# Kernel optimization log

Hardware: AMD Instinct MI355X
Metric: run time of the kernel (lower is better)

Reference implementation:

```python
import jax, jax.numpy as jnp
import numpy as np
import math

H = 768      # hidden_size
NH = 12      # num_head
DH = H // NH # head dim
FF = 4 * H
EPS = 1e-6

def _layernorm(x, g, b):
    mu = jnp.mean(x, axis=-1, keepdims=True)
    var = jnp.mean(jnp.square(x - mu), axis=-1, keepdims=True)
    return (x - mu) * jax.lax.rsqrt(var + EPS) * g + b

def setup_inputs() -> dict:
    key = jax.random.key(0)
    ks = jax.random.split(key, 16)
    B, N = 8, 1024
    xav = lambda k, i, o: jax.random.uniform(k, (i, o), jnp.float32, -1.0, 1.0) * math.sqrt(6.0 / (i + o))
    bias = lambda k, o: jax.random.normal(k, (o,), jnp.float32) * 1e-6
    return {
        "x": jax.random.normal(ks[0], (B, N, H), jnp.float32),
        "wq": xav(ks[1], H, H), "bq": bias(ks[2], H),
        "wk": xav(ks[3], H, H), "bk": bias(ks[4], H),
        "wv": xav(ks[5], H, H), "bv": bias(ks[6], H),
        "wo": xav(ks[7], H, H), "bo": bias(ks[8], H),
        "w1": xav(ks[9], H, FF), "b1": bias(ks[10], FF),
        "w2": xav(ks[11], FF, H), "b2": bias(ks[12], H),
        "g1": jnp.ones((H,), jnp.float32), "be1": jnp.zeros((H,), jnp.float32),
        "g2": jnp.ones((H,), jnp.float32), "be2": jnp.zeros((H,), jnp.float32),
    }

def reference(x, wq, bq, wk, bk, wv, bv, wo, bo, w1, b1, w2, b2, g1, be1, g2, be2):
    B, N, _ = x.shape
    x1 = _layernorm(x, g1, be1)
    # QKV projections -> (B, NH, N, DH)
    split = lambda t: t.reshape(B, N, NH, DH).transpose(0, 2, 1, 3)
    q = split(x1 @ wq + bq)
    k = split(x1 @ wk + bk)
    v = split(x1 @ wv + bv)
    # NOTE: original divides by sqrt(attention_size)=sqrt(H), not sqrt(DH)
    scores = jnp.einsum("bhqd,bhkd->bhqk", q, k) / math.sqrt(H)
    weights = jax.nn.softmax(scores, axis=-1)
    ctx = jnp.einsum("bhqk,bhkd->bhqd", weights, v)
    ctx = ctx.transpose(0, 2, 1, 3).reshape(B, N, H)
    attn_out = ctx @ wo + bo  # dropout is identity in eval
    x = x + attn_out
    x2 = _layernorm(x, g2, be2)
    h = jax.nn.gelu(x2 @ w1 + b1, approximate=False)  # torch F.gelu is exact erf gelu
    mlp_out = h @ w2 + b2
    x = x + mlp_out
    return (x, weights)
```

## Files before the change

kernel.cpp:

```cpp
#include <hip/hip_runtime.h>
#include <cstdint>
#include <cstddef>

#define H 768
#define NHEAD 12
#define DH 64
#define FFD 3072
#define BATCH 8
#define SEQ 1024
#define NTOK (BATCH*SEQ)
#define QKVS 2304

typedef __bf16 bf16x8 __attribute__((ext_vector_type(8)));
typedef float  floatx4 __attribute__((ext_vector_type(4)));

#define MFMA_BF16(a,b,c) __builtin_amdgcn_mfma_f32_16x16x32_bf16((a),(b),(c),0,0,0)

__device__ __forceinline__ void gload16(const void* g, void* l) {
    __builtin_amdgcn_global_load_lds((const __attribute__((address_space(1))) void*)g,
                                     (__attribute__((address_space(3))) void*)l,
                                     16, 0, 0);
}

__device__ __forceinline__ float gelu_erf(float x) {
    float z = fabsf(x) * 0.70710678118654752f;
    float t = __builtin_amdgcn_rcpf(1.0f + 0.3275911f * z);
    float poly = t * (0.254829592f +
               t * (-0.284496736f +
               t * (1.421413741f +
               t * (-1.453152027f +
               t * 1.061405429f))));
    float e = __expf(-z * z);
    float erfv = 1.0f - poly * e;
    erfv = copysignf(erfv, x);
    return 0.5f * x * (1.0f + erfv);
}

__global__ __launch_bounds__(256) void prep_kernel(
    const float* __restrict__ wq, const float* __restrict__ wk,
    const float* __restrict__ wv, const float* __restrict__ wo,
    const float* __restrict__ w1, const float* __restrict__ w2,
    const float* __restrict__ bq, const float* __restrict__ bk,
    const float* __restrict__ bv,
    __bf16* __restrict__ wqkvT, __bf16* __restrict__ woT,
    __bf16* __restrict__ w1T, __bf16* __restrict__ w2T,
    float* __restrict__ bqkv,
    const float* __restrict__ x, const float* __restrict__ g1,
    const float* __restrict__ be1, __bf16* __restrict__ x1b) {
    __shared__ float tile[32][33];
    int bid = blockIdx.x;
    int tid = threadIdx.x;
    if (bid < 6912) {
        const float* W; __bf16* T; int Kd, Nn, bx, by;
        if (bid < 1728) {
            int part = bid / 576;
            int rem = bid - part * 576;
            W = part == 0 ? wq : (part == 1 ? wk : wv);
            T = wqkvT + (size_t)part * H * H;
            Kd = H; Nn = H; bx = rem % 24; by = rem / 24;
        } else if (bid < 2304) {
            int rem = bid - 1728;
            W = wo; T = woT; Kd = H; Nn = H; bx = rem % 24; by = rem / 24;
        } else if (bid < 4608) {
            int rem = bid - 2304;
            W = w1; T = w1T; Kd = H; Nn = FFD; bx = rem % 96; by = rem / 96;
        } else {
            int rem = bid - 4608;
            W = w2; T = w2T; Kd = FFD; Nn = H; bx = rem % 24; by = rem / 24;
        }
        int tx = tid & 31, ty = tid >> 5;
        int n0 = bx * 32, k0 = by * 32;
#pragma unroll
        for (int i = 0; i < 32; i += 8)
            tile[ty + i][tx] = W[(size_t)(k0 + ty + i) * Nn + n0 + tx];
        __syncthreads();
#pragma unroll
        for (int i = 0; i < 32; i += 8)
            T[(size_t)(n0 + ty + i) * Kd + k0 + tx] = (__bf16)tile[tx][ty + i];
    } else if (bid < 6921) {
        int i = (bid - 6912) * 256 + tid;
        float v = i < H ? bq[i] : (i < 2 * H ? bk[i - H] : bv[i - 2 * H]);
        bqkv[i] = v;
    } else {
        int row  = (bid - 6921) * 4 + (tid >> 6);
        int lane = tid & 63;
        const float* xr = x + (size_t)row * H;
        float v[12];
        float s = 0.f;
#pragma unroll
        for (int i = 0; i < 12; i++) { v[i] = xr[lane + i * 64]; s += v[i]; }
#pragma unroll
        for (int m = 32; m >= 1; m >>= 1) s += __shfl_xor(s, m, 64);
        float mu = s * (1.0f / H);
        float q = 0.f;
#pragma unroll
        for (int i = 0; i < 12; i++) { float d = v[i] - mu; q += d * d; }
#pragma unroll
        for (int m = 32; m >= 1; m >>= 1) q += __shfl_xor(q, m, 64);
        float rstd = rsqrtf(q * (1.0f / H) + 1e-6f);
        __bf16* orow = x1b + (size_t)row * H;
#pragma unroll
        for (int i = 0; i < 12; i++) {
            int c = lane + i * 64;
            orow[c] = (__bf16)((v[i] - mu) * rstd * g1[c] + be1[c]);
        }
    }
}

__global__ __launch_bounds__(256) void ln_kernel(const float* __restrict__ x,
                                                 const float* __restrict__ g,
                                                 const float* __restrict__ be,
                                                 __bf16* __restrict__ out) {
    int row  = blockIdx.x * 4 + (threadIdx.x >> 6);
    int lane = threadIdx.x & 63;
    const float* xr = x + (size_t)row * H;
    float v[12];
    float s = 0.f;
#pragma unroll
    for (int i = 0; i < 12; i++) { v[i] = xr[lane + i * 64]; s += v[i]; }
#pragma unroll
    for (int m = 32; m >= 1; m >>= 1) s += __shfl_xor(s, m, 64);
    float mu = s * (1.0f / H);
    float q = 0.f;
#pragma unroll
    for (int i = 0; i < 12; i++) { float d = v[i] - mu; q += d * d; }
#pragma unroll
    for (int m = 32; m >= 1; m >>= 1) q += __shfl_xor(q, m, 64);
    float rstd = rsqrtf(q * (1.0f / H) + 1e-6f);
    __bf16* orow = out + (size_t)row * H;
#pragma unroll
    for (int i = 0; i < 12; i++) {
        int c = lane + i * 64;
        orow[c] = (__bf16)((v[i] - mu) * rstd * g[c] + be[c]);
    }
}

__global__ __launch_bounds__(256) void vtrans_kernel(const __bf16* __restrict__ qkv,
                                                     __bf16* __restrict__ vT) {
    __shared__ __bf16 tile[64][65];
    int b = blockIdx.z, h = blockIdx.y, n0 = blockIdx.x * 64;
    int tx = threadIdx.x, ty = threadIdx.y;
#pragma unroll
    for (int r = ty; r < 64; r += 4)
        tile[r][tx] = qkv[((size_t)b * SEQ + n0 + r) * QKVS + 2 * H + h * DH + tx];
    __syncthreads();
#pragma unroll
    for (int c = ty; c < 64; c += 4)
        vT[(((size_t)b * NHEAD + h) * DH + c) * SEQ + n0 + tx] = tile[tx][c];
}

template<bool GELU, bool HAS_RES, bool OUT_BF16>
__global__ __launch_bounds__(256) void gemm_kernel(const __bf16* __restrict__ A,
                                                   const __bf16* __restrict__ Bt,
                                                   const float* __restrict__ bias,
                                                   const float* __restrict__ res,
                                                   __bf16* __restrict__ obf,
                                                   float* __restrict__ ofp,
                                                   int Nn, int K) {
    __shared__ __bf16 As[128 * 32];
    __shared__ __bf16 Bs[128 * 32];
    int tid = threadIdx.x;
    int wave = tid >> 6, lane = tid & 63;
    int wr = wave >> 1, wc = wave & 1;
    int l15 = lane & 15, quad = lane >> 4;

    floatx4 acc[4][4];
    floatx4 zero = {0.f, 0.f, 0.f, 0.f};
#pragma unroll
    for (int i = 0; i < 4; i++)
#pragma unroll
        for (int j = 0; j < 4; j++) acc[i][j] = zero;

    int c0 = wave * 2, c1 = c0 + 1;
    int lr = lane >> 2, lc = (lane & 3) * 8;
    const __bf16* Ag0 = A + (size_t)(blockIdx.y * 128 + c0 * 16 + lr) * K + lc;
    const __bf16* Ag1 = A + (size_t)(blockIdx.y * 128 + c1 * 16 + lr) * K + lc;
    const __bf16* Bg0 = Bt + (size_t)(blockIdx.x * 128 + c0 * 16 + lr) * K + lc;
    const __bf16* Bg1 = Bt + (size_t)(blockIdx.x * 128 + c1 * 16 + lr) * K + lc;
    __bf16* AsD0 = &As[c0 * 512];
    __bf16* AsD1 = &As[c1 * 512];
    __bf16* BsD0 = &Bs[c0 * 512];
    __bf16* BsD1 = &Bs[c1 * 512];

    for (int k0 = 0; k0 < K; k0 += 32) {
        gload16(Ag0 + k0, AsD0);
        gload16(Ag1 + k0, AsD1);
        gload16(Bg0 + k0, BsD0);
        gload16(Bg1 + k0, BsD1);
        __syncthreads();
        bf16x8 af[4], bfv[4];
#pragma unroll
        for (int i = 0; i < 4; i++)
            af[i] = *(const bf16x8*)&As[(wr * 64 + i * 16 + l15) * 32 + quad * 8];
#pragma unroll
        for (int j = 0; j < 4; j++)
            bfv[j] = *(const bf16x8*)&Bs[(wc * 64 + j * 16 + l15) * 32 + quad * 8];
#pragma unroll
        for (int i = 0; i < 4; i++)
#pragma unroll
            for (int j = 0; j < 4; j++)
                acc[i][j] = MFMA_BF16(af[i], bfv[j], acc[i][j]);
        __syncthreads();
    }

#pragma unroll
    for (int i = 0; i < 4; i++) {
        int row = blockIdx.y * 128 + wr * 64 + i * 16 + quad * 4;
#pragma unroll
        for (int j = 0; j < 4; j++) {
            int col = blockIdx.x * 128 + wc * 64 + j * 16 + l15;
            float bsv = bias[col];
#pragma unroll
            for (int r = 0; r < 4; r++) {
                float vv = acc[i][j][r] + bsv;
                if (GELU) vv = gelu_erf(vv);
                if (HAS_RES) vv += res[(size_t)(row + r) * Nn + col];
                if (OUT_BF16) obf[(size_t)(row + r) * Nn + col] = (__bf16)vv;
                else          ofp[(size_t)(row + r) * Nn + col] = vv;
            }
        }
    }
}

__device__ __forceinline__ int sbidx(int row, int col) {
    return row * 1024 + (col ^ ((row & 7) << 3));
}

__global__ __launch_bounds__(256, 4) void attn_kernel(const __bf16* __restrict__ qkv,
                                                      const __bf16* __restrict__ vT,
                                                      float* __restrict__ Wout,
                                                      __bf16* __restrict__ ctx) {
    __shared__ __bf16 Sb[16 * 1024];
    __shared__ __align__(16) float red[2][16][4];
    int tid = threadIdx.x;
    int wave = tid >> 6, lane = tid & 63, l15 = lane & 15, quad = lane >> 4;

    int linear = blockIdx.x + 64 * (blockIdx.y + 12 * blockIdx.z);
    int xcd = linear & 7;
    int j   = linear >> 3;
    int bh  = xcd + 8 * (j >> 6);
    int rt  = j & 63;
    int h = bh % NHEAD, b = bh / NHEAD;

    const size_t tokbase = (size_t)b * SEQ * QKVS + h * DH;
    const float scale = 0.03608439182435161f;

    const __bf16* qrow = qkv + tokbase + (size_t)(rt * 16 + l15) * QKVS;
    bf16x8 qf0 = *(const bf16x8*)(qrow + quad * 8);
    bf16x8 qf1 = *(const bf16x8*)(qrow + 32 + quad * 8);

    floatx4 s[16];
    const __bf16* kbase = qkv + tokbase + H;
#pragma unroll
    for (int i = 0; i < 16; i++) {
        int ct = wave * 16 + i;
        const __bf16* krow = kbase + (size_t)(ct * 16 + l15) * QKVS;
        bf16x8 kf0 = *(const bf16x8*)(krow + quad * 8);
        bf16x8 kf1 = *(const bf16x8*)(krow + 32 + quad * 8);
        floatx4 a = {0.f, 0.f, 0.f, 0.f};
        a = MFMA_BF16(qf0, kf0, a);
        a = MFMA_BF16(qf1, kf1, a);
#pragma unroll
        for (int r = 0; r < 4; r++) s[i][r] = a[r] * scale;
    }

    float m4[4];
#pragma unroll
    for (int r = 0; r < 4; r++) {
        float m = s[0][r];
#pragma unroll
        for (int i = 1; i < 16; i++) m = fmaxf(m, s[i][r]);
#pragma unroll
        for (int msk = 8; msk >= 1; msk >>= 1) m = fmaxf(m, __shfl_xor(m, msk, 64));
        m4[r] = m;
    }
    if (l15 == 0) {
#pragma unroll
        for (int r = 0; r < 4; r++) red[0][quad * 4 + r][wave] = m4[r];
    }
    __syncthreads();
    float mrow[4];
#pragma unroll
    for (int r = 0; r < 4; r++) {
        float4 rr = *(const float4*)&red[0][quad * 4 + r][0];
        mrow[r] = fmaxf(fmaxf(rr.x, rr.y), fmaxf(rr.z, rr.w));
    }

    float s4[4] = {0.f, 0.f, 0.f, 0.f};
#pragma unroll
    for (int i = 0; i < 16; i++) {
#pragma unroll
        for (int r = 0; r < 4; r++) {
            float e = __expf(s[i][r] - mrow[r]);
            s[i][r] = e;
            s4[r] += e;
        }
    }
#pragma unroll
    for (int r = 0; r < 4; r++) {
#pragma unroll
        for (int msk = 8; msk >= 1; msk >>= 1) s4[r] += __shfl_xor(s4[r], msk, 64);
    }
    if (l15 == 0) {
#pragma unroll
        for (int r = 0; r < 4; r++) red[1][quad * 4 + r][wave] = s4[r];
    }
    __syncthreads();
    float inv[4];
#pragma unroll
    for (int r = 0; r < 4; r++) {
        float4 rr = *(const float4*)&red[1][quad * 4 + r][0];
        inv[r] = 1.0f / (rr.x + rr.y + rr.z + rr.w);
    }

    size_t wbase = (((size_t)b * NHEAD + h) * SEQ + rt * 16) * SEQ;
#pragma unroll
    for (int i = 0; i < 16; i++) {
        int col = (wave * 16 + i) * 16 + l15;
#pragma unroll
        for (int r = 0; r < 4; r++) {
            float w = s[i][r] * inv[r];
            int row = quad * 4 + r;
            __builtin_nontemporal_store(w, &Wout[wbase + (size_t)row * SEQ + col]);
            Sb[sbidx(row, col)] = (__bf16)w;
        }
    }
    __syncthreads();

    floatx4 acc = {0.f, 0.f, 0.f, 0.f};
    const __bf16* vbase = vT + (((size_t)b * NHEAD + h) * DH + wave * 16 + l15) * SEQ;
#pragma unroll
    for (int c = 0; c < 32; c++) {
        int k0 = c * 32 + quad * 8;
        bf16x8 af = *(const bf16x8*)&Sb[sbidx(l15, k0)];
        bf16x8 bv = *(const bf16x8*)(vbase + k0);
        acc = MFMA_BF16(af, bv, acc);
    }
#pragma unroll
    for (int r = 0; r < 4; r++)
        ctx[((size_t)b * SEQ + rt * 16 + quad * 4 + r) * H + h * DH + wave * 16 + l15] =
            (__bf16)acc[r];
}

extern "C" void kernel_launch(void* const* d_in, const int* in_sizes, int n_in,
                              void* d_out, int out_size, void* d_ws, size_t ws_size,
                              hipStream_t stream) {
    const float* x   = (const float*)d_in[0];
    const float* wq  = (const float*)d_in[1];
    const float* bq  = (const float*)d_in[2];
    const float* wk  = (const float*)d_in[3];
    const float* bk  = (const float*)d_in[4];
    const float* wv  = (const float*)d_in[5];
    const float* bv  = (const float*)d_in[6];
    const float* wo  = (const float*)d_in[7];
    const float* bo  = (const float*)d_in[8];
    const float* w1  = (const float*)d_in[9];
    const float* b1  = (const float*)d_in[10];
    const float* w2  = (const float*)d_in[11];
    const float* b2  = (const float*)d_in[12];
    const float* g1  = (const float*)d_in[13];
    const float* be1 = (const float*)d_in[14];
    const float* g2  = (const float*)d_in[15];
    const float* be2 = (const float*)d_in[16];

    char* ws = (char*)d_ws;
    const size_t SZB = (size_t)NTOK * H * 2;
    __bf16* x1b  = (__bf16*)(ws);
    __bf16* qkvb = (__bf16*)(ws + SZB);
    __bf16* vTb  = (__bf16*)(ws + 4 * SZB);
    __bf16* ctxb = (__bf16*)(ws + 5 * SZB);
    __bf16* x2b  = (__bf16*)(ws + 6 * SZB);
    __bf16* hb   = (__bf16*)(ws + 7 * SZB);
    size_t off = 7 * SZB + (size_t)NTOK * FFD * 2;
    float* xattn = (float*)(ws + off); off += (size_t)NTOK * H * 4;
    __bf16* wqkvT = (__bf16*)(ws + off); off += (size_t)3 * H * H * 2;
    __bf16* woT  = (__bf16*)(ws + off); off += (size_t)H * H * 2;
    __bf16* w1T  = (__bf16*)(ws + off); off += (size_t)H * FFD * 2;
    __bf16* w2T  = (__bf16*)(ws + off); off += (size_t)FFD * H * 2;
    float* bqkv  = (float*)(ws + off); off += (size_t)3 * H * 4;

    float* outx = (float*)d_out;
    float* outw = (float*)d_out + (size_t)NTOK * H;

    prep_kernel<<<8969, 256, 0, stream>>>(wq, wk, wv, wo, w1, w2, bq, bk, bv,
                                          wqkvT, woT, w1T, w2T, bqkv,
                                          x, g1, be1, x1b);

    gemm_kernel<false, false, true><<<dim3(QKVS / 128, NTOK / 128), 256, 0, stream>>>(
        x1b, wqkvT, bqkv, nullptr, qkvb, nullptr, QKVS, H);

    vtrans_kernel<<<dim3(16, NHEAD, BATCH), dim3(64, 4), 0, stream>>>(qkvb, vTb);

    attn_kernel<<<dim3(64, NHEAD, BATCH), 256, 0, stream>>>(qkvb, vTb, outw, ctxb);

    gemm_kernel<false, true, false><<<dim3(H / 128, NTOK / 128), 256, 0, stream>>>(
        ctxb, woT, bo, x, nullptr, xattn, H, H);

    ln_kernel<<<NTOK / 4, 256, 0, stream>>>(xattn, g2, be2, x2b);

    gemm_kernel<true, false, true><<<dim3(FFD / 128, NTOK / 128), 256, 0, stream>>>(
        x2b, w1T, b1, nullptr, hb, nullptr, FFD, H);

    gemm_kernel<false, true, false><<<dim3(H / 128, NTOK / 128), 256, 0, stream>>>(
        hb, w2T, b2, xattn, nullptr, outx, H, FFD);
}
```

Baseline: 851.3 us.

## Double GEMM K-tile to 64 with XOR-swizzled LDS layout

The GEMM main loop now stages a 128x64 K-slice of A and B per iteration instead of 128x32. That halves the number of barrier pairs and global-to-LDS issue rounds per output tile. The LDS layout uses an XOR swizzle of the 16-byte column chunk by row index, which is meant to avoid bank conflicts on the wider 128-byte rows. LDS use doubles to 32 KB per block, which may lower occupancy, and there is still no double buffering.

```diff
diff --git a/kernel.cpp b/kernel.cpp
--- a/kernel.cpp
+++ b/kernel.cpp
@@ -157,8 +157,8 @@
                                                    __bf16* __restrict__ obf,
                                                    float* __restrict__ ofp,
                                                    int Nn, int K) {
-    __shared__ __bf16 As[128 * 32];
-    __shared__ __bf16 Bs[128 * 32];
+    __shared__ __bf16 As[128 * 64];
+    __shared__ __bf16 Bs[128 * 64];
     int tid = threadIdx.x;
     int wave = tid >> 6, lane = tid & 63;
     int wr = wave >> 1, wc = wave & 1;
@@ -171,35 +171,45 @@
 #pragma unroll
         for (int j = 0; j < 4; j++) acc[i][j] = zero;
 
-    int c0 = wave * 2, c1 = c0 + 1;
-    int lr = lane >> 2, lc = (lane & 3) * 8;
-    const __bf16* Ag0 = A + (size_t)(blockIdx.y * 128 + c0 * 16 + lr) * K + lc;
-    const __bf16* Ag1 = A + (size_t)(blockIdx.y * 128 + c1 * 16 + lr) * K + lc;
-    const __bf16* Bg0 = Bt + (size_t)(blockIdx.x * 128 + c0 * 16 + lr) * K + lc;
-    const __bf16* Bg1 = Bt + (size_t)(blockIdx.x * 128 + c1 * 16 + lr) * K + lc;
-    __bf16* AsD0 = &As[c0 * 512];
-    __bf16* AsD1 = &As[c1 * 512];
-    __bf16* BsD0 = &Bs[c0 * 512];
-    __bf16* BsD1 = &Bs[c1 * 512];
-
-    for (int k0 = 0; k0 < K; k0 += 32) {
-        gload16(Ag0 + k0, AsD0);
-        gload16(Ag1 + k0, AsD1);
-        gload16(Bg0 + k0, BsD0);
-        gload16(Bg1 + k0, BsD1);
+    int lrow = lane >> 3;
+    int lcol = ((lane & 7) ^ lrow) * 8;
+    const __bf16* Agc[4];
+    const __bf16* Bgc[4];
+    __bf16* AsDc[4];
+    __bf16* BsDc[4];
+#pragma unroll
+    for (int cc = 0; cc < 4; cc++) {
+        int chunk = wave * 4 + cc;
+        int row = chunk * 8 + lrow;
+        Agc[cc] = A + (size_t)(blockIdx.y * 128 + row) * K + lcol;
+        Bgc[cc] = Bt + (size_t)(blockIdx.x * 128 + row) * K + lcol;
+        AsDc[cc] = &As[chunk * 512];
+        BsDc[cc] = &Bs[chunk * 512];
+    }
+
+    for (int k0 = 0; k0 < K; k0 += 64) {
+#pragma unroll
+        for (int cc = 0; cc < 4; cc++) {
+            gload16(Agc[cc] + k0, AsDc[cc]);
+            gload16(Bgc[cc] + k0, BsDc[cc]);
+        }
         __syncthreads();
-        bf16x8 af[4], bfv[4];
-#pragma unroll
-        for (int i = 0; i < 4; i++)
-            af[i] = *(const bf16x8*)&As[(wr * 64 + i * 16 + l15) * 32 + quad * 8];
-#pragma unroll
-        for (int j = 0; j < 4; j++)
-            bfv[j] = *(const bf16x8*)&Bs[(wc * 64 + j * 16 + l15) * 32 + quad * 8];
-#pragma unroll
-        for (int i = 0; i < 4; i++)
+#pragma unroll
+        for (int kk = 0; kk < 2; kk++) {
+            int c16 = (kk * 4 + quad) ^ (l15 & 7);
+            bf16x8 af[4], bfv[4];
+#pragma unroll
+            for (int i = 0; i < 4; i++)
+                af[i] = *(const bf16x8*)&As[(wr * 64 + i * 16 + l15) * 64 + c16 * 8];
 #pragma unroll
             for (int j = 0; j < 4; j++)
-                acc[i][j] = MFMA_BF16(af[i], bfv[j], acc[i][j]);
+                bfv[j] = *(const bf16x8*)&Bs[(wc * 64 + j * 16 + l15) * 64 + c16 * 8];
+#pragma unroll
+            for (int i = 0; i < 4; i++)
+#pragma unroll
+                for (int j = 0; j < 4; j++)
+                    acc[i][j] = MFMA_BF16(af[i], bfv[j], acc[i][j]);
+        }
         __syncthreads();
     }
 
```

New measurement: 825.3 us. -3.1%, faster.
